# Performance work log

Hardware: AMD Instinct MI355X
Metric: run time of the kernel (lower is better)

Reference implementation:

```python
import jax, jax.numpy as jnp
import numpy as np

B, H, W, C = 32, 56, 56, 256
NH, WS, SH = 8, 7, 3
HD = C // NH
SCALE = HD ** -0.5
N = WS * WS
MLP = 4 * C


def _rel_pos_index():
    coords = np.stack(np.meshgrid(np.arange(WS), np.arange(WS), indexing='ij')).reshape(2, -1)
    rel = (coords[:, :, None] - coords[:, None, :]).transpose(1, 2, 0)
    rel[..., 0] += WS - 1
    rel[..., 1] += WS - 1
    rel[..., 0] *= 2 * WS - 1
    return jnp.asarray(rel.sum(-1))  # (N, N) int


def _attn_mask():
    # standard Swin shifted-window mask, computed statically
    img = np.zeros((H, W))
    cnt = 0
    for hs in (slice(0, -WS), slice(-WS, -SH), slice(-SH, None)):
        for ws_ in (slice(0, -WS), slice(-WS, -SH), slice(-SH, None)):
            img[hs, ws_] = cnt
            cnt += 1
    mw = img.reshape(H // WS, WS, W // WS, WS).transpose(0, 2, 1, 3).reshape(-1, N)
    am = mw[:, None, :] - mw[:, :, None]
    am = np.where(am != 0, -1e9, 0.0).astype(np.float32)
    return jnp.asarray(am)  # (nW, N, N)


def _part(x):
    b = x.shape[0]
    x = x.reshape(b, H // WS, WS, W // WS, WS, C)
    return x.transpose(0, 1, 3, 2, 4, 5).reshape(-1, N, C)


def _rev(xw):
    x = xw.reshape(-1, H // WS, W // WS, WS, WS, C)
    return x.transpose(0, 1, 3, 2, 4, 5).reshape(-1, H, W, C)


def _ln(x, g, b):
    m = x.mean(-1, keepdims=True)
    v = x.var(-1, keepdims=True)
    return (x - m) / jnp.sqrt(v + 1e-5) * g + b


def setup_inputs() -> dict:
    key = jax.random.key(0)
    ks = jax.random.split(key, 6)
    s = 0.02
    return {
        'x': jax.random.normal(ks[0], (B, H, W, C), jnp.float32),
        'gamma1': jnp.ones((C,), jnp.float32),
        'beta1': jnp.zeros((C,), jnp.float32),
        'w_qkv': jax.random.normal(ks[1], (C, 3 * C), jnp.float32) * s,
        'b_qkv': jnp.zeros((3 * C,), jnp.float32),
        'rpb': jax.random.normal(ks[2], ((2 * WS - 1) ** 2, NH), jnp.float32) * s,
        'w_proj': jax.random.normal(ks[3], (C, C), jnp.float32) * s,
        'b_proj': jnp.zeros((C,), jnp.float32),
        'gamma2': jnp.ones((C,), jnp.float32),
        'beta2': jnp.zeros((C,), jnp.float32),
        'w_fc1': jax.random.normal(ks[4], (C, MLP), jnp.float32) * s,
        'b_fc1': jnp.zeros((MLP,), jnp.float32),
        'w_fc2': jax.random.normal(ks[5], (MLP, C), jnp.float32) * s,
        'b_fc2': jnp.zeros((C,), jnp.float32),
    }


def reference(x, gamma1, beta1, w_qkv, b_qkv, rpb, w_proj, b_proj, gamma2, beta2, w_fc1, b_fc1, w_fc2, b_fc2):
    idx = _rel_pos_index()
    mask = _attn_mask()  # (nW, N, N)
    nW = mask.shape[0]

    shortcut = x
    xn = _ln(x, gamma1, beta1)
    xs = jnp.roll(xn, (-SH, -SH), axis=(1, 2))        # cyclic shift
    xw = _part(xs)                                     # (B*nW, N, C)

    qkv = (xw @ w_qkv + b_qkv).reshape(-1, N, 3, NH, HD).transpose(2, 0, 3, 1, 4)
    # SNN-variant IF (ReLU) gates on q, k, v
    q, k, v = jax.nn.relu(qkv[0]), jax.nn.relu(qkv[1]), jax.nn.relu(qkv[2])

    attn = jnp.einsum('bhnd,bhmd->bhnm', q * SCALE, k)  # (B*nW, NH, N, N)
    bias = rpb[idx].transpose(2, 0, 1)                  # (NH, N, N)
    attn = attn + bias[None]
    attn = attn.reshape(-1, nW, NH, N, N) + mask[None, :, None]
    attn = attn.reshape(-1, NH, N, N)
    # stdp_qk ReLU before softmax (faithful to source)
    attn = jax.nn.softmax(jax.nn.relu(attn), axis=-1)
    # stdp_av ReLU on attention output
    out = jax.nn.relu(jnp.einsum('bhnm,bhmd->bhnd', attn, v))
    out = out.transpose(0, 2, 1, 3).reshape(-1, N, C) @ w_proj + b_proj

    xs = _rev(out)
    x = shortcut + jnp.roll(xs, (SH, SH), axis=(1, 2))  # reverse shift + residual

    h = jax.nn.gelu(_ln(x, gamma2, beta2) @ w_fc1 + b_fc1, approximate=False)
    return x + h @ w_fc2 + b_fc2
```

## Files before the change

### kernel.cpp

```cpp
#include <hip/hip_runtime.h>
#include <stdint.h>

typedef unsigned short u16;
typedef short bf16x8 __attribute__((ext_vector_type(8)));
typedef float f32x4 __attribute__((ext_vector_type(4)));

#define NTOK 100352
#define NWIN 2048
#define CC 256
#define NHEAD 8
#define HDIM 32
#define NWT 49
#define MLPD 1024
#define ATT_SCALE 0.17677669529663687f

__device__ __forceinline__ u16 f2b(float f) {
  union { float f; uint32_t u; } c; c.f = f;
  return (u16)((c.u + 0x7fffu + ((c.u >> 16) & 1u)) >> 16);
}
__device__ __forceinline__ float b2f(u16 h) {
  union { uint32_t u; float f; } c; c.u = ((uint32_t)h) << 16;
  return c.f;
}
__device__ __forceinline__ uint32_t f2b2(float lo, float hi) {
  uint32_t r;
  asm("v_cvt_pk_bf16_f32 %0, %1, %2" : "=v"(r) : "v"(lo), "v"(hi));
  return r;
}

__device__ __forceinline__ void gload_lds16(const void* g, void* l) {
  __builtin_amdgcn_global_load_lds((const __attribute__((address_space(1))) void*)g,
                                   (__attribute__((address_space(3))) void*)l, 16, 0, 0);
}

__global__ __launch_bounds__(256)
void prep_k(const float* __restrict__ wqkv, const float* __restrict__ wproj,
            const float* __restrict__ wfc1, const float* __restrict__ wfc2,
            const float* __restrict__ rpb,
            u16* __restrict__ qkvT, u16* __restrict__ projT,
            u16* __restrict__ fc1T, u16* __restrict__ fc2T, float* __restrict__ lut) {
  int i = blockIdx.x * 256 + threadIdx.x;
  if (i < 196608) {
    int k = i / 768, n = i % 768;
    qkvT[(size_t)n * 256 + k] = f2b(wqkv[i]);
  } else if (i < 262144) {
    int j = i - 196608, k = j / 256, n = j % 256;
    projT[(size_t)n * 256 + k] = f2b(wproj[j]);
  } else if (i < 524288) {
    int j = i - 262144, k = j / 1024, n = j % 1024;
    fc1T[(size_t)n * 256 + k] = f2b(wfc1[j]);
  } else if (i < 786432) {
    int j = i - 524288, k = j / 256, n = j % 256;
    fc2T[(size_t)n * 1024 + k] = f2b(wfc2[j]);
  } else if (i < 819200) {
    int j = i - 786432;
    int h = j >> 12, m = (j >> 6) & 63, n = j & 63;
    float v = 0.f;
    if (m < 49 && n < 49) {
      int i1 = n / 7, j1 = n % 7, i2 = m / 7, j2 = m % 7;
      v = rpb[((i1 - i2 + 6) * 13 + (j1 - j2 + 6)) * 8 + h];
    }
    lut[j] = v;
  }
}

__global__ __launch_bounds__(256)
void ln_k(const float* __restrict__ x, const float* __restrict__ g,
          const float* __restrict__ be, u16* __restrict__ out) {
  int token = blockIdx.x * 4 + (threadIdx.x >> 6);
  int lane = threadIdx.x & 63;
  int win = token / 49, nn = token % 49;
  int b = win >> 6, wh = (win >> 3) & 7, ww = win & 7;
  int i = nn / 7, j = nn % 7;
  int h = wh * 7 + i + 3; if (h >= 56) h -= 56;
  int w = ww * 7 + j + 3; if (w >= 56) w -= 56;
  size_t src = ((size_t)((b * 56 + h) * 56 + w)) * CC;
  f32x4 v = *(const f32x4*)&x[src + lane * 4];
  float s1 = v[0] + v[1] + v[2] + v[3];
  float s2 = v[0]*v[0] + v[1]*v[1] + v[2]*v[2] + v[3]*v[3];
#pragma unroll
  for (int o = 32; o; o >>= 1) { s1 += __shfl_xor(s1, o); s2 += __shfl_xor(s2, o); }
  float mean = s1 * (1.f / 256.f);
  float var = s2 * (1.f / 256.f) - mean * mean;
  float rstd = rsqrtf(var + 1e-5f);
  f32x4 gv = *(const f32x4*)&g[lane * 4];
  f32x4 bv = *(const f32x4*)&be[lane * 4];
  float y0 = (v[0]-mean)*rstd*gv[0] + bv[0];
  float y1 = (v[1]-mean)*rstd*gv[1] + bv[1];
  float y2 = (v[2]-mean)*rstd*gv[2] + bv[2];
  float y3 = (v[3]-mean)*rstd*gv[3] + bv[3];
  *(uint2*)&out[(size_t)token * CC + lane * 4] = make_uint2(f2b2(y0, y1), f2b2(y2, y3));
}

#define BM 128
#define BN 128
enum { EPI_QKV = 0 };

template<int EPI, int NKT>
__global__ __launch_bounds__(256)
void gemm_k(const u16* __restrict__ A, const u16* __restrict__ BT,
            const float* __restrict__ bias,
            void* __restrict__ p0, const void* __restrict__ p1) {
  constexpr int K = NKT * 64;
  __shared__ u16 aL[2][BM * 64];
  __shared__ u16 bL[BN * 64];
  const int tid = threadIdx.x;
  const int lane = tid & 63;
  const int wv = tid >> 6;
  const int wm = wv >> 1, wn = wv & 1;

  int bx = blockIdx.x, by = blockIdx.y;
  {
    int nwg = gridDim.x * gridDim.y;
    int lin = by * gridDim.x + bx;
    int q = nwg >> 3, r = nwg & 7;
    int xcd = lin & 7, idx = lin >> 3;
    int wg = (xcd < r ? xcd * (q + 1) : r * (q + 1) + (xcd - r) * q) + idx;
    bx = wg % gridDim.x;
    by = wg / gridDim.x;
  }
  const long m0 = (long)by * BM;
  const int n0 = bx * BN;

  f32x4 acc[4][4] = {};
  const int r15 = lane & 15;
  const int g4 = lane >> 4;

  const u16* pA[4];
  const u16* pB[4];
  int lslot[4];
#pragma unroll
  for (int it = 0; it < 4; ++it) {
    int slot = tid + 256 * it;
    int row = slot >> 3, c8 = slot & 7;
    int cs = c8 ^ (row & 7);
    pA[it] = &A[(m0 + row) * K + cs * 8];
    pB[it] = &BT[(size_t)(n0 + row) * K + cs * 8];
    lslot[it] = slot * 8;
  }
  int aoff[2][4], boff[2][4];
#pragma unroll
  for (int kk = 0; kk < 2; ++kk)
#pragma unroll
    for (int m = 0; m < 4; ++m) {
      int rowa = wm * 64 + m * 16 + r15;
      aoff[kk][m] = rowa * 64 + (((kk * 4 + g4) ^ (rowa & 7)) << 3);
      int rowb = wn * 64 + m * 16 + r15;
      boff[kk][m] = rowb * 64 + (((kk * 4 + g4) ^ (rowb & 7)) << 3);
    }

  auto stageA = [&](int bufi) {
#pragma unroll
    for (int it = 0; it < 4; ++it) { gload_lds16(pA[it], &aL[bufi][lslot[it]]); pA[it] += 64; }
  };
  auto stageB = [&]() {
#pragma unroll
    for (int it = 0; it < 4; ++it) { gload_lds16(pB[it], &bL[lslot[it]]); pB[it] += 64; }
  };

  stageB();
  stageA(0);
  stageA(1);

  for (int t = 0; t < NKT; ++t) {
    if (t + 1 < NKT) asm volatile("s_waitcnt vmcnt(4)" ::: "memory");
    else             asm volatile("s_waitcnt vmcnt(0)" ::: "memory");
    __builtin_amdgcn_sched_barrier(0);
    __builtin_amdgcn_s_barrier();
    __builtin_amdgcn_sched_barrier(0);
    {
      const u16* ab = aL[t & 1];
#pragma unroll
      for (int kk = 0; kk < 2; ++kk) {
        bf16x8 af[4], bfr[4];
#pragma unroll
        for (int m = 0; m < 4; ++m) af[m] = *(const bf16x8*)&ab[aoff[kk][m]];
#pragma unroll
        for (int n = 0; n < 4; ++n) bfr[n] = *(const bf16x8*)&bL[boff[kk][n]];
#pragma unroll
        for (int n = 0; n < 4; ++n)
#pragma unroll
          for (int m = 0; m < 4; ++m)
            acc[n][m] = __builtin_amdgcn_mfma_f32_16x16x32_bf16(bfr[n], af[m], acc[n][m], 0, 0, 0);
      }
    }
    __builtin_amdgcn_sched_barrier(0);
    __builtin_amdgcn_s_barrier();
    __builtin_amdgcn_sched_barrier(0);
    if (t + 1 < NKT) stageB();
    if (t + 2 < NKT) stageA(t & 1);
  }

#pragma unroll
  for (int mt = 0; mt < 4; ++mt) {
    const int mrow = (int)m0 + wm * 64 + mt * 16 + r15;
    int win = mrow / 49, nn = mrow - win * 49;
#pragma unroll
    for (int nt = 0; nt < 4; ++nt) {
      const int col0 = n0 + wn * 64 + nt * 16 + g4 * 4;
      f32x4 bv = *(const f32x4*)&bias[col0];
      f32x4 v;
#pragma unroll
      for (int j = 0; j < 4; ++j) v[j] = acc[nt][mt][j] + bv[j];
      int s = col0 >> 8, head = (col0 >> 5) & 7, d0 = col0 & 31;
      float sc = (s == 0) ? ATT_SCALE : 1.f;
#pragma unroll
      for (int j = 0; j < 4; ++j) v[j] = fmaxf(v[j], 0.f) * sc;
      u16* dst = (u16*)p0 + (size_t)s * ((size_t)NTOK * CC);
      *(uint2*)&dst[(((size_t)(win * NHEAD + head)) * NWT + nn) * HDIM + d0] =
          make_uint2(f2b2(v[0], v[1]), f2b2(v[2], v[3]));
    }
  }
}

__global__ __launch_bounds__(512)
void gemm_ln_k(const u16* __restrict__ A, const u16* __restrict__ BT,
               const float* __restrict__ bias, const float* __restrict__ xres,
               const float* __restrict__ g2, const float* __restrict__ be2,
               u16* __restrict__ x2, u16* __restrict__ xn2) {
  constexpr int K = 256;
  constexpr int NKT = 4;
  __shared__ u16 aL[2][128 * 64];
  __shared__ u16 bL[256 * 64];
  __shared__ float st[4 * 128 * 2];
  const int tid = threadIdx.x;
  const int lane = tid & 63;
  const int wv = tid >> 6;
  const int wm = wv >> 2;
  const int wn = wv & 3;
  const int r15 = lane & 15;
  const int g4 = lane >> 4;

  int by = blockIdx.x;
  {
    int nwg = gridDim.x;
    int q = nwg >> 3, r = nwg & 7;
    int xcd = by & 7, idx = by >> 3;
    by = (xcd < r ? xcd * (q + 1) : r * (q + 1) + (xcd - r) * q) + idx;
  }
  const long m0 = (long)by * 128;

  f32x4 acc[4][4] = {};

  const u16* pA[2];
  int la[2];
#pragma unroll
  for (int it = 0; it < 2; ++it) {
    int slot = tid + 512 * it;
    int row = slot >> 3, c8 = slot & 7;
    int cs = c8 ^ (row & 7);
    pA[it] = &A[(m0 + row) * K + cs * 8];
    la[it] = slot * 8;
  }
  const u16* pB[4];
  int lb[4];
#pragma unroll
  for (int it = 0; it < 4; ++it) {
    int slot = tid + 512 * it;
    int row = slot >> 3, c8 = slot & 7;
    int cs = c8 ^ (row & 7);
    pB[it] = &BT[(size_t)row * K + cs * 8];
    lb[it] = slot * 8;
  }
  int aoff[2][4], boff[2][4];
#pragma unroll
  for (int kk = 0; kk < 2; ++kk)
#pragma unroll
    for (int m = 0; m < 4; ++m) {
      int rowa = wm * 64 + m * 16 + r15;
      aoff[kk][m] = rowa * 64 + (((kk * 4 + g4) ^ (rowa & 7)) << 3);
      int rowb = wn * 64 + m * 16 + r15;
      boff[kk][m] = rowb * 64 + (((kk * 4 + g4) ^ (rowb & 7)) << 3);
    }

  auto stageA = [&](int bufi) {
#pragma unroll
    for (int it = 0; it < 2; ++it) { gload_lds16(pA[it], &aL[bufi][la[it]]); pA[it] += 64; }
  };
  auto stageB = [&]() {
#pragma unroll
    for (int it = 0; it < 4; ++it) { gload_lds16(pB[it], &bL[lb[it]]); pB[it] += 64; }
  };

  stageB();
  stageA(0);
  stageA(1);

  for (int t = 0; t < NKT; ++t) {
    if (t + 1 < NKT) asm volatile("s_waitcnt vmcnt(2)" ::: "memory");
    else             asm volatile("s_waitcnt vmcnt(0)" ::: "memory");
    __builtin_amdgcn_sched_barrier(0);
    __builtin_amdgcn_s_barrier();
    __builtin_amdgcn_sched_barrier(0);
    {
      const u16* ab = aL[t & 1];
#pragma unroll
      for (int kk = 0; kk < 2; ++kk) {
        bf16x8 af[4], bfr[4];
#pragma unroll
        for (int m = 0; m < 4; ++m) af[m] = *(const bf16x8*)&ab[aoff[kk][m]];
#pragma unroll
        for (int n = 0; n < 4; ++n) bfr[n] = *(const bf16x8*)&bL[boff[kk][n]];
#pragma unroll
        for (int n = 0; n < 4; ++n)
#pragma unroll
          for (int m = 0; m < 4; ++m)
            acc[n][m] = __builtin_amdgcn_mfma_f32_16x16x32_bf16(bfr[n], af[m], acc[n][m], 0, 0, 0);
      }
    }
    __builtin_amdgcn_sched_barrier(0);
    __builtin_amdgcn_s_barrier();
    __builtin_amdgcn_sched_barrier(0);
    if (t + 1 < NKT) stageB();
    if (t + 2 < NKT) stageA(t & 1);
  }

  size_t pix[4];
  float s1[4] = {}, s2[4] = {};
#pragma unroll
  for (int mt = 0; mt < 4; ++mt) {
    const int mrow = (int)m0 + wm * 64 + mt * 16 + r15;
    int win = mrow / 49, nn = mrow - win * 49;
    int b = win >> 6, wh = (win >> 3) & 7, ww = win & 7;
    int i = nn / 7, jj = nn - i * 7;
    int h = wh * 7 + i + 3; if (h >= 56) h -= 56;
    int w = ww * 7 + jj + 3; if (w >= 56) w -= 56;
    pix[mt] = (size_t)((b * 56 + h) * 56 + w);
#pragma unroll
    for (int nt = 0; nt < 4; ++nt) {
      const int col0 = wn * 64 + nt * 16 + g4 * 4;
      f32x4 bv = *(const f32x4*)&bias[col0];
      f32x4 r = *(const f32x4*)&xres[pix[mt] * CC + col0];
      f32x4 v;
#pragma unroll
      for (int j = 0; j < 4; ++j) {
        v[j] = acc[nt][mt][j] + bv[j] + r[j];
        s1[mt] += v[j];
        s2[mt] += v[j] * v[j];
      }
      *(uint2*)&x2[(size_t)mrow * CC + col0] =
          make_uint2(f2b2(v[0], v[1]), f2b2(v[2], v[3]));
      acc[nt][mt] = v;
    }
    s1[mt] += __shfl_xor(s1[mt], 16);  s1[mt] += __shfl_xor(s1[mt], 32);
    s2[mt] += __shfl_xor(s2[mt], 16);  s2[mt] += __shfl_xor(s2[mt], 32);
    if (g4 == 0) {
      int wrow = wm * 64 + mt * 16 + r15;
      st[(wn * 128 + wrow) * 2 + 0] = s1[mt];
      st[(wn * 128 + wrow) * 2 + 1] = s2[mt];
    }
  }
  __syncthreads();
#pragma unroll
  for (int mt = 0; mt < 4; ++mt) {
    const int mrow = (int)m0 + wm * 64 + mt * 16 + r15;
    int wrow = wm * 64 + mt * 16 + r15;
    float t1 = 0.f, t2 = 0.f;
#pragma unroll
    for (int w2 = 0; w2 < 4; ++w2) {
      t1 += st[(w2 * 128 + wrow) * 2 + 0];
      t2 += st[(w2 * 128 + wrow) * 2 + 1];
    }
    float mean = t1 * (1.f / 256.f);
    float var = t2 * (1.f / 256.f) - mean * mean;
    float rstd = rsqrtf(var + 1e-5f);
#pragma unroll
    for (int nt = 0; nt < 4; ++nt) {
      const int col0 = wn * 64 + nt * 16 + g4 * 4;
      f32x4 gv = *(const f32x4*)&g2[col0];
      f32x4 bv = *(const f32x4*)&be2[col0];
      float y0 = (acc[nt][mt][0] - mean) * rstd * gv[0] + bv[0];
      float y1 = (acc[nt][mt][1] - mean) * rstd * gv[1] + bv[1];
      float y2 = (acc[nt][mt][2] - mean) * rstd * gv[2] + bv[2];
      float y3 = (acc[nt][mt][3] - mean) * rstd * gv[3] + bv[3];
      *(uint2*)&xn2[(size_t)mrow * CC + col0] = make_uint2(f2b2(y0, y1), f2b2(y2, y3));
    }
  }
}

__global__ __launch_bounds__(512, 4)
void mlp_fused_k(const u16* __restrict__ xn, const u16* __restrict__ fc1T,
                 const u16* __restrict__ fc2T, const float* __restrict__ b1,
                 const float* __restrict__ b2v, const u16* __restrict__ x2,
                 float* __restrict__ outp) {
  __shared__ u16 lds[24576];
  u16* shA0 = lds;
  u16* shA1 = lds + 4096;
  u16* shB1 = lds + 8192;
  u16* shB2 = lds;
  u16* shH  = lds + 16384;

  const int tid = threadIdx.x;
  const int lane = tid & 63;
  const int wv = tid >> 6;
  const int wmw = wv >> 2;
  const int wnw = wv & 3;
  const int r15 = lane & 15;
  const int g4 = lane >> 4;

  int by = blockIdx.x;
  {
    int nwg = gridDim.x;
    int q = nwg >> 3, r = nwg & 7;
    int xcd = by & 7, idx = by >> 3;
    by = (xcd < r ? xcd * (q + 1) : r * (q + 1) + (xcd - r) * q) + idx;
  }
  const long m0 = (long)by * 64;

  const int rowA = tid >> 3, csA = (tid & 7) ^ (rowA & 7);
  const u16* pAbase = &xn[(m0 + rowA) * 256 + csA * 8];
  int rowB1[2], lb1[2];
  const u16* pB1base[2];
#pragma unroll
  for (int it = 0; it < 2; ++it) {
    int slot = tid + 512 * it;
    rowB1[it] = slot >> 3;
    int cs = (slot & 7) ^ (rowB1[it] & 7);
    pB1base[it] = &fc1T[(size_t)rowB1[it] * 256 + cs * 8];
    lb1[it] = slot * 8;
  }
  int lb2[4];
  const u16* pB2base[4];
#pragma unroll
  for (int it = 0; it < 4; ++it) {
    int slot = tid + 512 * it;
    int row = slot >> 3;
    int cs = (slot & 7) ^ (row & 7);
    pB2base[it] = &fc2T[(size_t)row * 1024 + cs * 8];
    lb2[it] = slot * 8;
  }

  int a1off[2][2], b1off[2][2];
#pragma unroll
  for (int kk = 0; kk < 2; ++kk)
#pragma unroll
    for (int m = 0; m < 2; ++m) {
      int ra = wmw * 32 + m * 16 + r15;
      a1off[kk][m] = ra * 64 + (((kk * 4 + g4) ^ (ra & 7)) << 3);
      int rb = wnw * 32 + m * 16 + r15;
      b1off[kk][m] = rb * 64 + (((kk * 4 + g4) ^ (rb & 7)) << 3);
    }
  int b2off[2][4];
#pragma unroll
  for (int kk = 0; kk < 2; ++kk)
#pragma unroll
    for (int n = 0; n < 4; ++n) {
      int rb = wnw * 64 + n * 16 + r15;
      b2off[kk][n] = rb * 64 + (((kk * 4 + g4) ^ (rb & 7)) << 3);
    }

  f32x4 oacc[4][2] = {};

  for (int hc = 0; hc < 8; ++hc) {
    const size_t b1chunk = (size_t)hc * 128 * 256;
    gload_lds16(pB1base[0] + b1chunk, &shB1[lb1[0]]);
    gload_lds16(pB1base[1] + b1chunk, &shB1[lb1[1]]);
    gload_lds16(pAbase,      &shA0[tid * 8]);
    gload_lds16(pAbase + 64, &shA1[tid * 8]);

    f32x4 acc1[2][2] = {};
    for (int t = 0; t < 4; ++t) {
      if (t + 1 < 4) asm volatile("s_waitcnt vmcnt(1)" ::: "memory");
      else           asm volatile("s_waitcnt vmcnt(0)" ::: "memory");
      __builtin_amdgcn_sched_barrier(0);
      __builtin_amdgcn_s_barrier();
      __builtin_amdgcn_sched_barrier(0);
      {
        const u16* ab = (t & 1) ? shA1 : shA0;
#pragma unroll
        for (int kk = 0; kk < 2; ++kk) {
          bf16x8 af[2], bfr[2];
#pragma unroll
          for (int m = 0; m < 2; ++m) af[m] = *(const bf16x8*)&ab[a1off[kk][m]];
#pragma unroll
          for (int n = 0; n < 2; ++n) bfr[n] = *(const bf16x8*)&shB1[b1off[kk][n]];
#pragma unroll
          for (int n = 0; n < 2; ++n)
#pragma unroll
            for (int m = 0; m < 2; ++m)
              acc1[n][m] = __builtin_amdgcn_mfma_f32_16x16x32_bf16(bfr[n], af[m], acc1[n][m], 0, 0, 0);
        }
      }
      __builtin_amdgcn_sched_barrier(0);
      __builtin_amdgcn_s_barrier();
      __builtin_amdgcn_sched_barrier(0);
      if (t + 1 < 4) {
        gload_lds16(pB1base[0] + b1chunk + (t + 1) * 64, &shB1[lb1[0]]);
        gload_lds16(pB1base[1] + b1chunk + (t + 1) * 64, &shB1[lb1[1]]);
      }
      if (t + 2 < 4) {
        u16* dst = (t & 1) ? shA1 : shA0;
        gload_lds16(pAbase + (t + 2) * 64, &dst[tid * 8]);
      }
    }
    gload_lds16(pB2base[0] + hc * 128, &shB2[lb2[0]]);
    gload_lds16(pB2base[1] + hc * 128, &shB2[lb2[1]]);
    gload_lds16(pB2base[2] + hc * 128, &shB2[lb2[2]]);
    gload_lds16(pB2base[3] + hc * 128, &shB2[lb2[3]]);

#pragma unroll
    for (int mt = 0; mt < 2; ++mt) {
      const int hrow = wmw * 32 + mt * 16 + r15;
#pragma unroll
      for (int nt = 0; nt < 2; ++nt) {
        const int col0 = wnw * 32 + nt * 16 + g4 * 4;
        f32x4 bv = *(const f32x4*)&b1[hc * 128 + col0];
        f32x4 v;
#pragma unroll
        for (int j = 0; j < 4; ++j) {
          float u = acc1[nt][mt][j] + bv[j];
          float t2 = 0.79788456f * (u + 0.044715f * u * u * u);
          float th = 1.f - 2.f / (__expf(2.f * t2) + 1.f);
          v[j] = 0.5f * u * (1.f + th);
        }
        int hidx = hrow * 128 + (((col0 >> 3) ^ (hrow & 15)) << 3) + (col0 & 4);
        *(uint2*)&shH[hidx] = make_uint2(f2b2(v[0], v[1]), f2b2(v[2], v[3]));
      }
    }
    asm volatile("s_waitcnt lgkmcnt(0)" ::: "memory");
    __builtin_amdgcn_sched_barrier(0);
    asm volatile("s_waitcnt vmcnt(0)" ::: "memory");
    __builtin_amdgcn_sched_barrier(0);
    __builtin_amdgcn_s_barrier();
    __builtin_amdgcn_sched_barrier(0);

#pragma unroll
    for (int kt = 0; kt < 2; ++kt) {
#pragma unroll
      for (int kk = 0; kk < 2; ++kk) {
        bf16x8 af[2], bfr[4];
#pragma unroll
        for (int m = 0; m < 2; ++m) {
          int hrow = wmw * 32 + m * 16 + r15;
          int kchunk = kt * 8 + kk * 4 + g4;
          af[m] = *(const bf16x8*)&shH[hrow * 128 + ((kchunk ^ (hrow & 15)) << 3)];
        }
#pragma unroll
        for (int n = 0; n < 4; ++n) bfr[n] = *(const bf16x8*)&shB2[b2off[kk][n]];
#pragma unroll
        for (int n = 0; n < 4; ++n)
#pragma unroll
          for (int m = 0; m < 2; ++m)
            oacc[n][m] = __builtin_amdgcn_mfma_f32_16x16x32_bf16(bfr[n], af[m], oacc[n][m], 0, 0, 0);
      }
      __builtin_amdgcn_sched_barrier(0);
      __builtin_amdgcn_s_barrier();
      __builtin_amdgcn_sched_barrier(0);
      if (kt == 0) {
        gload_lds16(pB2base[0] + hc * 128 + 64, &shB2[lb2[0]]);
        gload_lds16(pB2base[1] + hc * 128 + 64, &shB2[lb2[1]]);
        gload_lds16(pB2base[2] + hc * 128 + 64, &shB2[lb2[2]]);
        gload_lds16(pB2base[3] + hc * 128 + 64, &shB2[lb2[3]]);
        asm volatile("s_waitcnt vmcnt(0)" ::: "memory");
        __builtin_amdgcn_sched_barrier(0);
        __builtin_amdgcn_s_barrier();
        __builtin_amdgcn_sched_barrier(0);
      }
    }
  }

#pragma unroll
  for (int mt = 0; mt < 2; ++mt) {
    const int mrow = (int)m0 + wmw * 32 + mt * 16 + r15;
    int win = mrow / 49, nn = mrow - win * 49;
    int b = win >> 6, wh = (win >> 3) & 7, ww = win & 7;
    int i = nn / 7, jj = nn - i * 7;
    int h = wh * 7 + i + 3; if (h >= 56) h -= 56;
    int w = ww * 7 + jj + 3; if (w >= 56) w -= 56;
    size_t pix = (size_t)((b * 56 + h) * 56 + w);
#pragma unroll
    for (int nt = 0; nt < 4; ++nt) {
      const int col0 = wnw * 64 + nt * 16 + g4 * 4;
      f32x4 bv = *(const f32x4*)&b2v[col0];
      f32x4 v;
#pragma unroll
      for (int j = 0; j < 4; ++j) v[j] = oacc[nt][mt][j] + bv[j];
      uint2 rb = *(const uint2*)&x2[(size_t)mrow * CC + col0];
      v[0] += b2f((u16)(rb.x & 0xffffu));
      v[1] += b2f((u16)(rb.x >> 16));
      v[2] += b2f((u16)(rb.y & 0xffffu));
      v[3] += b2f((u16)(rb.y >> 16));
      *(f32x4*)&outp[pix * CC + col0] = v;
    }
  }
}

__global__ __launch_bounds__(256)
void attn_mfma_k(const u16* __restrict__ q, const u16* __restrict__ k2,
                 const u16* __restrict__ v2, const float* __restrict__ lut,
                 u16* __restrict__ out) {
  __shared__ u16 P_lds[4][64 * 72];
  const int tid = threadIdx.x;
  const int wv = tid >> 6;
  const int lane = tid & 63;
  const int c = lane & 15;
  const int g = lane >> 4;
  const int blk = blockIdx.x * 4 + wv;
  const int head = blk & 7;
  const int win = blk >> 3;
  const int wimg = win & 63;
  const int wh = wimg >> 3, ww = wimg & 7;
  const size_t base = (size_t)blk * (NWT * HDIM);
  u16* Pw = P_lds[wv];

  bf16x8 kf[4], qf[4];
#pragma unroll
  for (int t = 0; t < 4; ++t) {
    kf[t] = *(const bf16x8*)&k2[base + (size_t)(t * 16 + c) * HDIM + g * 8];
    qf[t] = *(const bf16x8*)&q [base + (size_t)(t * 16 + c) * HDIM + g * 8];
  }
  bf16x8 vf[2][2];
#pragma unroll
  for (int kcc = 0; kcc < 2; ++kcc)
#pragma unroll
    for (int td = 0; td < 2; ++td)
#pragma unroll
      for (int jj = 0; jj < 8; ++jj) {
        int m = kcc * 32 + g * 8 + jj;
        m = m < 49 ? m : 48;
        vf[kcc][td][jj] = (short)v2[base + (size_t)m * HDIM + td * 16 + c];
      }

  f32x4 acc[4][4] = {};
#pragma unroll
  for (int tm = 0; tm < 4; ++tm)
#pragma unroll
    for (int tn = 0; tn < 4; ++tn)
      acc[tm][tn] = __builtin_amdgcn_mfma_f32_16x16x32_bf16(kf[tm], qf[tn], acc[tm][tn], 0, 0, 0);

  const float* lrow = &lut[(size_t)head * 64 * 64];
  int Ln[4];
#pragma unroll
  for (int tn = 0; tn < 4; ++tn) {
    int n = tn * 16 + c;
    int i1 = (n * 9363) >> 16;
    int j1 = n - i1 * 7;
    int rh = (wh < 7) ? 0 : (i1 < 4 ? 1 : 2);
    int rw = (ww < 7) ? 0 : (j1 < 4 ? 1 : 2);
    Ln[tn] = rh * 3 + rw;
  }
  float colmax[4] = {0.f, 0.f, 0.f, 0.f};
#pragma unroll
  for (int tm = 0; tm < 4; ++tm)
#pragma unroll
    for (int j = 0; j < 4; ++j) {
      int m = tm * 16 + g * 4 + j;
      int i2 = (m * 9363) >> 16;
      int j2 = m - i2 * 7;
      int rh = (wh < 7) ? 0 : (i2 < 4 ? 1 : 2);
      int rw = (ww < 7) ? 0 : (j2 < 4 ? 1 : 2);
      int Lm = rh * 3 + rw;
#pragma unroll
      for (int tn = 0; tn < 4; ++tn) {
        float s = acc[tm][tn][j] + lrow[m * 64 + tn * 16 + c];
        s = fmaxf(s, 0.f);
        if (Lm != Ln[tn]) s = 0.f;
        acc[tm][tn][j] = s;
        colmax[tn] = fmaxf(colmax[tn], s);
      }
    }
#pragma unroll
  for (int tn = 0; tn < 4; ++tn) {
    colmax[tn] = fmaxf(colmax[tn], __shfl_xor(colmax[tn], 16));
    colmax[tn] = fmaxf(colmax[tn], __shfl_xor(colmax[tn], 32));
  }
  float colsum[4] = {0.f, 0.f, 0.f, 0.f};
#pragma unroll
  for (int tm = 0; tm < 4; ++tm)
#pragma unroll
    for (int j = 0; j < 4; ++j) {
      int m = tm * 16 + g * 4 + j;
      bool mvalid = (m < NWT);
#pragma unroll
      for (int tn = 0; tn < 4; ++tn) {
        float e = mvalid ? __expf(acc[tm][tn][j] - colmax[tn]) : 0.f;
        acc[tm][tn][j] = e;
        colsum[tn] += e;
      }
    }
#pragma unroll
  for (int tn = 0; tn < 4; ++tn) {
    colsum[tn] += __shfl_xor(colsum[tn], 16);
    colsum[tn] += __shfl_xor(colsum[tn], 32);
    colsum[tn] = 1.f / colsum[tn];
  }

#pragma unroll
  for (int tn = 0; tn < 4; ++tn) {
    int n = tn * 16 + c;
#pragma unroll
    for (int tm = 0; tm < 4; ++tm) {
      float r = colsum[tn];
      *(uint2*)&Pw[n * 72 + tm * 16 + g * 4] =
          make_uint2(f2b2(acc[tm][tn][0] * r, acc[tm][tn][1] * r),
                     f2b2(acc[tm][tn][2] * r, acc[tm][tn][3] * r));
    }
  }

  f32x4 oacc[4][2] = {};
#pragma unroll
  for (int kcc = 0; kcc < 2; ++kcc) {
    bf16x8 pf[4];
#pragma unroll
    for (int tr = 0; tr < 4; ++tr)
      pf[tr] = *(const bf16x8*)&Pw[(tr * 16 + c) * 72 + kcc * 32 + g * 8];
#pragma unroll
    for (int tr = 0; tr < 4; ++tr)
#pragma unroll
      for (int td = 0; td < 2; ++td)
        oacc[tr][td] = __builtin_amdgcn_mfma_f32_16x16x32_bf16(pf[tr], vf[kcc][td], oacc[tr][td], 0, 0, 0);
  }

#pragma unroll
  for (int tr = 0; tr < 4; ++tr)
#pragma unroll
    for (int j = 0; j < 4; ++j) {
      int n = tr * 16 + g * 4 + j;
      if (n < NWT) {
#pragma unroll
        for (int td = 0; td < 2; ++td) {
          int d = td * 16 + c;
          out[((size_t)(win * NWT + n)) * CC + head * HDIM + d] =
              f2b(fmaxf(oacc[tr][td][j], 0.f));
        }
      }
    }
}

extern "C" void kernel_launch(void* const* d_in, const int* in_sizes, int n_in,
                              void* d_out, int out_size, void* d_ws, size_t ws_size,
                              hipStream_t stream) {
  const float* x      = (const float*)d_in[0];
  const float* gamma1 = (const float*)d_in[1];
  const float* beta1  = (const float*)d_in[2];
  const float* w_qkv  = (const float*)d_in[3];
  const float* b_qkv  = (const float*)d_in[4];
  const float* rpb    = (const float*)d_in[5];
  const float* w_proj = (const float*)d_in[6];
  const float* b_proj = (const float*)d_in[7];
  const float* gamma2 = (const float*)d_in[8];
  const float* beta2  = (const float*)d_in[9];
  const float* w_fc1  = (const float*)d_in[10];
  const float* b_fc1  = (const float*)d_in[11];
  const float* w_fc2  = (const float*)d_in[12];
  const float* b_fc2  = (const float*)d_in[13];
  float* out = (float*)d_out;

  char* ws = (char*)d_ws;
  size_t off = 0;
  auto alloc = [&](size_t bytes) { void* p = ws + off; off = (off + bytes + 255) & ~(size_t)255; return p; };

  u16* wqkvT = (u16*)alloc(768 * 256 * 2);
  u16* wprojT = (u16*)alloc(256 * 256 * 2);
  u16* wfc1T = (u16*)alloc(1024 * 256 * 2);
  u16* wfc2T = (u16*)alloc(256 * 1024 * 2);
  float* lut = (float*)alloc(8 * 64 * 64 * 4);
  u16* region2 = (u16*)alloc((size_t)NTOK * CC * 2);
  char* region1 = (char*)alloc((size_t)3 * NTOK * CC * 2);

  u16* xw = region2;
  u16* qb = (u16*)region1;
  u16* kb = qb + (size_t)NTOK * CC;
  u16* vb = kb + (size_t)NTOK * CC;
  u16* attn_out = region2;
  u16* x2 = (u16*)region1;
  u16* xn2 = x2 + (size_t)NTOK * CC;

  if (ws_size < off) return;

  prep_k<<<3200, 256, 0, stream>>>(w_qkv, w_proj, w_fc1, w_fc2, rpb,
                                   wqkvT, wprojT, wfc1T, wfc2T, lut);

  ln_k<<<NTOK / 4, 256, 0, stream>>>(x, gamma1, beta1, xw);

  gemm_k<EPI_QKV, 4><<<dim3(768 / BN, NTOK / BM), 256, 0, stream>>>(
      xw, wqkvT, b_qkv, (void*)qb, nullptr);

  attn_mfma_k<<<NWIN * NHEAD / 4, 256, 0, stream>>>(qb, kb, vb, lut, attn_out);

  gemm_ln_k<<<NTOK / 128, 512, 0, stream>>>(
      attn_out, wprojT, b_proj, x, gamma2, beta2, x2, xn2);

  mlp_fused_k<<<NTOK / 64, 512, 0, stream>>>(
      xn2, wfc1T, wfc2T, b_fc1, b_fc2, x2, out);
}
```

Baseline: 480.1 us.

## Widen fused MLP hidden chunk to 256 and simplify GELU evaluation

The fused MLP kernel now processes the hidden dimension in 4 chunks of 256 instead of 8 chunks of 128. This halves the number of chunk iterations, each with its own reloads of the xn A tile and its barriers. LDS grows from 48KB to 80KB per block, which may reduce occupancy below the launch_bounds target of 4. The tanh-GELU is also rewritten as u*sigmoid using exp2 and a hardware reciprocal, which cuts VALU work per element.

```diff
diff --git a/kernel.cpp b/kernel.cpp
--- a/kernel.cpp
+++ b/kernel.cpp
@@ -383,12 +383,12 @@
                  const u16* __restrict__ fc2T, const float* __restrict__ b1,
                  const float* __restrict__ b2v, const u16* __restrict__ x2,
                  float* __restrict__ outp) {
-  __shared__ u16 lds[24576];
+  __shared__ u16 lds[40960];
   u16* shA0 = lds;
   u16* shA1 = lds + 4096;
   u16* shB1 = lds + 8192;
   u16* shB2 = lds;
-  u16* shH  = lds + 16384;
+  u16* shH  = lds + 24576;
 
   const int tid = threadIdx.x;
   const int lane = tid & 63;
@@ -409,14 +409,14 @@
 
   const int rowA = tid >> 3, csA = (tid & 7) ^ (rowA & 7);
   const u16* pAbase = &xn[(m0 + rowA) * 256 + csA * 8];
-  int rowB1[2], lb1[2];
-  const u16* pB1base[2];
-#pragma unroll
-  for (int it = 0; it < 2; ++it) {
+  int lb1[4];
+  const u16* pB1base[4];
+#pragma unroll
+  for (int it = 0; it < 4; ++it) {
     int slot = tid + 512 * it;
-    rowB1[it] = slot >> 3;
-    int cs = (slot & 7) ^ (rowB1[it] & 7);
-    pB1base[it] = &fc1T[(size_t)rowB1[it] * 256 + cs * 8];
+    int row = slot >> 3;
+    int cs = (slot & 7) ^ (row & 7);
+    pB1base[it] = &fc1T[(size_t)row * 256 + cs * 8];
     lb1[it] = slot * 8;
   }
   int lb2[4];
@@ -430,16 +430,20 @@
     lb2[it] = slot * 8;
   }
 
-  int a1off[2][2], b1off[2][2];
-#pragma unroll
-  for (int kk = 0; kk < 2; ++kk)
+  int a1off[2][2], b1off[2][4];
+#pragma unroll
+  for (int kk = 0; kk < 2; ++kk) {
 #pragma unroll
     for (int m = 0; m < 2; ++m) {
       int ra = wmw * 32 + m * 16 + r15;
       a1off[kk][m] = ra * 64 + (((kk * 4 + g4) ^ (ra & 7)) << 3);
-      int rb = wnw * 32 + m * 16 + r15;
-      b1off[kk][m] = rb * 64 + (((kk * 4 + g4) ^ (rb & 7)) << 3);
-    }
+    }
+#pragma unroll
+    for (int n = 0; n < 4; ++n) {
+      int rb = wnw * 64 + n * 16 + r15;
+      b1off[kk][n] = rb * 64 + (((kk * 4 + g4) ^ (rb & 7)) << 3);
+    }
+  }
   int b2off[2][4];
 #pragma unroll
   for (int kk = 0; kk < 2; ++kk)
@@ -451,14 +455,16 @@
 
   f32x4 oacc[4][2] = {};
 
-  for (int hc = 0; hc < 8; ++hc) {
-    const size_t b1chunk = (size_t)hc * 128 * 256;
+  for (int hc2 = 0; hc2 < 4; ++hc2) {
+    const size_t b1chunk = (size_t)hc2 * 256 * 256;
     gload_lds16(pB1base[0] + b1chunk, &shB1[lb1[0]]);
     gload_lds16(pB1base[1] + b1chunk, &shB1[lb1[1]]);
+    gload_lds16(pB1base[2] + b1chunk, &shB1[lb1[2]]);
+    gload_lds16(pB1base[3] + b1chunk, &shB1[lb1[3]]);
     gload_lds16(pAbase,      &shA0[tid * 8]);
     gload_lds16(pAbase + 64, &shA1[tid * 8]);
 
-    f32x4 acc1[2][2] = {};
+    f32x4 acc1[4][2] = {};
     for (int t = 0; t < 4; ++t) {
       if (t + 1 < 4) asm volatile("s_waitcnt vmcnt(1)" ::: "memory");
       else           asm volatile("s_waitcnt vmcnt(0)" ::: "memory");
@@ -469,13 +475,13 @@
         const u16* ab = (t & 1) ? shA1 : shA0;
 #pragma unroll
         for (int kk = 0; kk < 2; ++kk) {
-          bf16x8 af[2], bfr[2];
+          bf16x8 af[2], bfr[4];
 #pragma unroll
           for (int m = 0; m < 2; ++m) af[m] = *(const bf16x8*)&ab[a1off[kk][m]];
 #pragma unroll
-          for (int n = 0; n < 2; ++n) bfr[n] = *(const bf16x8*)&shB1[b1off[kk][n]];
-#pragma unroll
-          for (int n = 0; n < 2; ++n)
+          for (int n = 0; n < 4; ++n) bfr[n] = *(const bf16x8*)&shB1[b1off[kk][n]];
+#pragma unroll
+          for (int n = 0; n < 4; ++n)
 #pragma unroll
             for (int m = 0; m < 2; ++m)
               acc1[n][m] = __builtin_amdgcn_mfma_f32_16x16x32_bf16(bfr[n], af[m], acc1[n][m], 0, 0, 0);
@@ -487,33 +493,36 @@
       if (t + 1 < 4) {
         gload_lds16(pB1base[0] + b1chunk + (t + 1) * 64, &shB1[lb1[0]]);
         gload_lds16(pB1base[1] + b1chunk + (t + 1) * 64, &shB1[lb1[1]]);
+        gload_lds16(pB1base[2] + b1chunk + (t + 1) * 64, &shB1[lb1[2]]);
+        gload_lds16(pB1base[3] + b1chunk + (t + 1) * 64, &shB1[lb1[3]]);
       }
       if (t + 2 < 4) {
         u16* dst = (t & 1) ? shA1 : shA0;
         gload_lds16(pAbase + (t + 2) * 64, &dst[tid * 8]);
       }
     }
-    gload_lds16(pB2base[0] + hc * 128, &shB2[lb2[0]]);
-    gload_lds16(pB2base[1] + hc * 128, &shB2[lb2[1]]);
-    gload_lds16(pB2base[2] + hc * 128, &shB2[lb2[2]]);
-    gload_lds16(pB2base[3] + hc * 128, &shB2[lb2[3]]);
+    gload_lds16(pB2base[0] + hc2 * 256, &shB2[lb2[0]]);
+    gload_lds16(pB2base[1] + hc2 * 256, &shB2[lb2[1]]);
+    gload_lds16(pB2base[2] + hc2 * 256, &shB2[lb2[2]]);
+    gload_lds16(pB2base[3] + hc2 * 256, &shB2[lb2[3]]);
 
 #pragma unroll
     for (int mt = 0; mt < 2; ++mt) {
       const int hrow = wmw * 32 + mt * 16 + r15;
 #pragma unroll
-      for (int nt = 0; nt < 2; ++nt) {
-        const int col0 = wnw * 32 + nt * 16 + g4 * 4;
-        f32x4 bv = *(const f32x4*)&b1[hc * 128 + col0];
+      for (int nt = 0; nt < 4; ++nt) {
+        const int col0 = wnw * 64 + nt * 16 + g4 * 4;
+        f32x4 bv = *(const f32x4*)&b1[hc2 * 256 + col0];
         f32x4 v;
 #pragma unroll
         for (int j = 0; j < 4; ++j) {
           float u = acc1[nt][mt][j] + bv[j];
-          float t2 = 0.79788456f * (u + 0.044715f * u * u * u);
-          float th = 1.f - 2.f / (__expf(2.f * t2) + 1.f);
-          v[j] = 0.5f * u * (1.f + th);
+          float u2 = u * u;
+          float tt = u * fmaf(0.044715f, u2, 1.f);
+          float e = exp2f(tt * -2.3022029f);
+          v[j] = u * __builtin_amdgcn_rcpf(1.f + e);
         }
-        int hidx = hrow * 128 + (((col0 >> 3) ^ (hrow & 15)) << 3) + (col0 & 4);
+        int hidx = hrow * 256 + (((col0 >> 3) ^ (hrow & 31)) << 3) + (col0 & 4);
         *(uint2*)&shH[hidx] = make_uint2(f2b2(v[0], v[1]), f2b2(v[2], v[3]));
       }
     }
@@ -525,7 +534,7 @@
     __builtin_amdgcn_sched_barrier(0);
 
 #pragma unroll
-    for (int kt = 0; kt < 2; ++kt) {
+    for (int kt = 0; kt < 4; ++kt) {
 #pragma unroll
       for (int kk = 0; kk < 2; ++kk) {
         bf16x8 af[2], bfr[4];
@@ -533,7 +542,7 @@
         for (int m = 0; m < 2; ++m) {
           int hrow = wmw * 32 + m * 16 + r15;
           int kchunk = kt * 8 + kk * 4 + g4;
-          af[m] = *(const bf16x8*)&shH[hrow * 128 + ((kchunk ^ (hrow & 15)) << 3)];
+          af[m] = *(const bf16x8*)&shH[hrow * 256 + ((kchunk ^ (hrow & 31)) << 3)];
         }
 #pragma unroll
         for (int n = 0; n < 4; ++n) bfr[n] = *(const bf16x8*)&shB2[b2off[kk][n]];
@@ -546,11 +555,11 @@
       __builtin_amdgcn_sched_barrier(0);
       __builtin_amdgcn_s_barrier();
       __builtin_amdgcn_sched_barrier(0);
-      if (kt == 0) {
-        gload_lds16(pB2base[0] + hc * 128 + 64, &shB2[lb2[0]]);
-        gload_lds16(pB2base[1] + hc * 128 + 64, &shB2[lb2[1]]);
-        gload_lds16(pB2base[2] + hc * 128 + 64, &shB2[lb2[2]]);
-        gload_lds16(pB2base[3] + hc * 128 + 64, &shB2[lb2[3]]);
+      if (kt + 1 < 4) {
+        gload_lds16(pB2base[0] + hc2 * 256 + (kt + 1) * 64, &shB2[lb2[0]]);
+        gload_lds16(pB2base[1] + hc2 * 256 + (kt + 1) * 64, &shB2[lb2[1]]);
+        gload_lds16(pB2base[2] + hc2 * 256 + (kt + 1) * 64, &shB2[lb2[2]]);
+        gload_lds16(pB2base[3] + hc2 * 256 + (kt + 1) * 64, &shB2[lb2[3]]);
         asm volatile("s_waitcnt vmcnt(0)" ::: "memory");
         __builtin_amdgcn_sched_barrier(0);
         __builtin_amdgcn_s_barrier();
```

Result: slower. 491.5 us (+2.4%).
